# Optimization experiments

Hardware: AMD Instinct MI355X
Metric: run time of the kernel (lower is better)

The kernel has to match this reference:

```python
import jax, jax.numpy as jnp
import numpy as np

N_NODES = 50000   # field_size == number of graph nodes
N_EDGES = 800000  # avg degree 16
VOCAB = 200000    # feature_size
EMB = 64          # embedding_size == in_dim
HID = 64          # num_hidden
SLOPE = 0.2       # leaky relu negative slope


def setup_inputs() -> dict:
    key = jax.random.key(0)
    ks = jax.random.split(key, 20)
    s = 0.05
    d = {}
    d["features"] = jax.random.randint(ks[0], (8, N_NODES), 0, VOCAB, dtype=jnp.int32)
    d["feature_values"] = jax.random.uniform(ks[1], (8, N_NODES), dtype=jnp.float32)
    d["src"] = jax.random.randint(ks[2], (N_EDGES,), 0, N_NODES, dtype=jnp.int32)
    d["dst"] = jax.random.randint(ks[3], (N_EDGES,), 0, N_NODES, dtype=jnp.int32)
    d["emb"] = jax.random.normal(ks[4], (VOCAB, EMB), jnp.float32) * s
    # layer 0: in=64 -> heads=2, out=64 (no residual)
    d["W0"]  = jax.random.normal(ks[5], (EMB, 2 * HID), jnp.float32) * s
    d["al0"] = jax.random.normal(ks[6], (2, HID), jnp.float32) * s
    d["ar0"] = jax.random.normal(ks[7], (2, HID), jnp.float32) * s
    d["b0"]  = jnp.zeros((2 * HID,), jnp.float32)
    # layer 1: in=128 -> heads=2, out=64 (identity residual since in == heads*out)
    d["W1"]  = jax.random.normal(ks[8], (2 * HID, 2 * HID), jnp.float32) * s
    d["al1"] = jax.random.normal(ks[9], (2, HID), jnp.float32) * s
    d["ar1"] = jax.random.normal(ks[10], (2, HID), jnp.float32) * s
    d["b1"]  = jnp.zeros((2 * HID,), jnp.float32)
    # output layer: in=128 -> heads=1, out=64 (projected residual), no activation
    d["W2"]    = jax.random.normal(ks[11], (2 * HID, EMB), jnp.float32) * s
    d["al2"]   = jax.random.normal(ks[12], (1, EMB), jnp.float32) * s
    d["ar2"]   = jax.random.normal(ks[13], (1, EMB), jnp.float32) * s
    d["b2"]    = jnp.zeros((EMB,), jnp.float32)
    d["resW2"] = jax.random.normal(ks[14], (2 * HID, EMB), jnp.float32) * s
    return d


def _gat_layer(h, src, dst, W, al, ar, b, res, act):
    """DGL-style GATConv. h: [N, in], W: [in, H*D], al/ar: [H, D]."""
    N = h.shape[0]
    H, D = al.shape
    fh = (h @ W).reshape(N, H, D)                      # [N, H, D]
    el = jnp.einsum('nhd,hd->nh', fh, al)              # [N, H]
    er = jnp.einsum('nhd,hd->nh', fh, ar)              # [N, H]
    e = jax.nn.leaky_relu(el[src] + er[dst], SLOPE)    # [E, H]
    # edge softmax grouped by destination node
    m = jax.ops.segment_max(e, dst, num_segments=N)
    m = jnp.where(jnp.isfinite(m), m, 0.0)
    ex = jnp.exp(e - m[dst])
    den = jax.ops.segment_sum(ex, dst, num_segments=N)
    alpha = ex / jnp.maximum(den[dst], 1e-9)           # [E, H]
    out = jax.ops.segment_sum(alpha[:, :, None] * fh[src], dst, num_segments=N)  # [N, H, D]
    if res is not None:
        out = out + res
    out = out + b.reshape(H, D)
    if act:
        out = jax.nn.elu(out)
    return out


def reference(features, feature_values, src, dst, emb,
              W0, al0, ar0, b0, W1, al1, ar1, b1,
              W2, al2, ar2, b2, resW2):
    # embedding lookup scaled by feature values: [B, field, emb]
    fe = emb[features] * feature_values[..., None]
    h = fe[0]                                          # [N_NODES, EMB]
    # layer 0: no residual, elu, flatten heads
    h = _gat_layer(h, src, dst, W0, al0, ar0, b0, None, True).reshape(N_NODES, -1)
    # layer 1: identity residual (in == heads*out), elu, flatten heads
    res1 = h.reshape(N_NODES, 2, HID)
    h = _gat_layer(h, src, dst, W1, al1, ar1, b1, res1, True).reshape(N_NODES, -1)
    # output layer: projected residual, no activation, mean over heads
    res2 = (h @ resW2).reshape(N_NODES, 1, EMB)
    logits = _gat_layer(h, src, dst, W2, al2, ar2, b2, res2, False).mean(axis=1)
    return logits
```

## Files before the change

kernel.cpp:

```cpp
#include <hip/hip_runtime.h>
#include <hip/hip_fp16.h>


typedef __attribute__((ext_vector_type(8))) short short8;
typedef __attribute__((ext_vector_type(4))) float float4v;

__device__ __forceinline__ float lrelu(float x){ return fmaxf(x, 0.2f*x); }

__device__ __forceinline__ unsigned short f2bf(float f){
  unsigned int u = __float_as_uint(f);
  u += 0x7fffu + ((u >> 16) & 1u);
  return (unsigned short)(u >> 16);
}
__device__ __forceinline__ unsigned short f2h(float f){
  return __half_as_ushort(__float2half(f));
}
__device__ __forceinline__ int bperm(int idx, int v){
  return __builtin_amdgcn_ds_bpermute(idx, v);
}
__device__ __forceinline__ float bperm_f(int idx, int v){
  return __int_as_float(__builtin_amdgcn_ds_bpermute(idx, v));
}
__device__ __forceinline__ float elu1(float x){
  return x > 0.f ? x : (__expf(x) - 1.f);
}

__global__ void k_zero_i32(int* __restrict__ p, int n){
  int i = blockIdx.x*blockDim.x + threadIdx.x;
  if (i < n) p[i] = 0;
}

__global__ void k_hist_rank(const int* __restrict__ dst, int* __restrict__ counts,
                            int* __restrict__ rank, int E){
  int i = blockIdx.x*blockDim.x + threadIdx.x;
  if (i < E){
    int d = dst[i];
    rank[i] = atomicAdd(&counts[d], 1);
  }
}

__global__ void k_scan_local(const int* __restrict__ counts, int* __restrict__ row_ptr,
                             int* __restrict__ bsum, int N){
  __shared__ int s[256];
  int t = threadIdx.x, g = blockIdx.x*256 + t;
  int v = (g < N) ? counts[g] : 0;
  s[t] = v; __syncthreads();
  #pragma unroll
  for (int off = 1; off < 256; off <<= 1){
    int x = 0;
    if (t >= off) x = s[t-off];
    __syncthreads();
    s[t] += x;
    __syncthreads();
  }
  if (g < N) row_ptr[g+1] = s[t];
  if (g == 0 && t == 0) row_ptr[0] = 0;
  if (t == 255) bsum[blockIdx.x] = s[255];
}

__global__ void k_scan_top(int* __restrict__ bsum, int nb){
  __shared__ int s[256];
  int t = threadIdx.x;
  int v = (t < nb) ? bsum[t] : 0;
  s[t] = v; __syncthreads();
  #pragma unroll
  for (int off = 1; off < 256; off <<= 1){
    int x = 0;
    if (t >= off) x = s[t-off];
    __syncthreads();
    s[t] += x;
    __syncthreads();
  }
  if (t < nb) bsum[t] = s[t] - v;
}

__global__ void k_scan_fix(int* __restrict__ row_ptr, const int* __restrict__ bsum, int N){
  int g = blockIdx.x*256 + threadIdx.x;
  if (g < N && blockIdx.x > 0) row_ptr[g+1] += bsum[blockIdx.x];
}

__global__ void k_scatter2(const int* __restrict__ src, const int* __restrict__ dst,
                           const int* __restrict__ rank, const int* __restrict__ row_ptr,
                           int* __restrict__ ssrc, int E){
  int i = blockIdx.x*blockDim.x + threadIdx.x;
  if (i < E) ssrc[row_ptr[dst[i]] + rank[i]] = src[i];
}

__global__ void k_wprep_all(const float* __restrict__ W0, const float* __restrict__ W1,
                            const float* __restrict__ W2, const float* __restrict__ rW2,
                            unsigned short* __restrict__ Wt0, unsigned short* __restrict__ Wt1,
                            unsigned short* __restrict__ Wt2){
  int id = blockIdx.x*256 + threadIdx.x;
  if (id < 128*64){
    int n = id/64, k = id%64;
    Wt0[n*64 + k] = f2bf(W0[k*128 + n]);
  } else if (id < 128*64 + 128*128){
    int i = id - 128*64; int n = i/128, k = i%128;
    Wt1[n*128 + k] = f2bf(W1[k*128 + n]);
  } else if (id < 128*64 + 2*128*128){
    int i = id - 128*64 - 128*128; int n = i/128, k = i%128;
    float v = (n < 64) ? W2[k*64 + n] : rW2[k*64 + (n - 64)];
    Wt2[n*128 + k] = f2bf(v);
  }
}

template<int IN, int H, bool EMBED>
__global__ __launch_bounds__(256) void k_gemm_mfma(
    const unsigned short* __restrict__ hb,
    const int* __restrict__ feat, const float* __restrict__ fv,
    const float* __restrict__ embp,
    const unsigned short* __restrict__ Wt,
    const float* __restrict__ al, const float* __restrict__ ar,
    unsigned short* __restrict__ fhb,
    float* __restrict__ elr, int N){
  constexpr int KS = IN/32;
  constexpr int LDP = IN + 8;
  __shared__ unsigned short Wt_s[128*LDP];
  const int t = threadIdx.x;
  const int lane = t & 63, wid = t >> 6;
  const int l15 = lane & 15, quad = lane >> 4;
  const int row0 = blockIdx.x*64 + wid*16;

  for (int id = t; id < 128*(IN/8); id += 256){
    int r = id/(IN/8), seg = id%(IN/8);
    ((uint4*)(Wt_s + r*LDP))[seg] = ((const uint4*)(Wt + (size_t)r*IN))[seg];
  }
  short8 a[KS];
  int arow = row0 + l15;
  if (EMBED){
    if (arow < N){
      const float* er2 = embp + (size_t)feat[arow]*64;
      float sc = fv[arow];
      #pragma unroll
// ... 41 lines not shown
  }
  #pragma unroll
  for (int reg = 0; reg < 4; reg++){
    int row = row0 + quad*4 + reg;
    bool rv = row < N;
    if (rv){
      #pragma unroll
      for (int nt = 0; nt < 8; nt++)
        fhb[(size_t)row*128 + nt*16 + l15] = f2h(acc[nt][reg]);
    }
    float pel0 = 0.f, per0 = 0.f, pel1 = 0.f, per1 = 0.f;
    #pragma unroll
    for (int nt = 0; nt < 4; nt++){
      pel0 += acc[nt][reg]*alc[nt];     per0 += acc[nt][reg]*arc[nt];
      pel1 += acc[nt+4][reg]*alc[nt+4]; per1 += acc[nt+4][reg]*arc[nt+4];
    }
    #pragma unroll
    for (int off = 1; off < 16; off <<= 1){
      pel0 += __shfl_xor(pel0, off, 64);
      pel1 += __shfl_xor(pel1, off, 64);
      per0 += __shfl_xor(per0, off, 64);
      per1 += __shfl_xor(per1, off, 64);
    }
    if (l15 == 0 && rv){
      elr[row*4+0] = pel0;
      elr[row*4+1] = (H == 2) ? pel1 : 0.f;
      elr[row*4+2] = per0;
      elr[row*4+3] = (H == 2) ? per1 : 0.f;
    }
  }
}

template<int H>
__global__ __launch_bounds__(256) void k_agg(
    const unsigned short* __restrict__ fhb,
    const float* __restrict__ elr,
    const int* __restrict__ row_ptr, const int* __restrict__ ssrc,
    const float* __restrict__ bias, const float* __restrict__ res,
    int act, int res_from_fh,
    float* __restrict__ out, int out_ld, unsigned* __restrict__ outb, int N){
  int lane = threadIdx.x & 63, wid = threadIdx.x >> 6;
  int n = blockIdx.x*4 + wid;
  if (n >= N) return;
  int beg = row_ptr[n], end = row_ptr[n+1];
  float er0 = elr[n*4+2];
  float er1 = (H == 2) ? elr[n*4+3] : 0.f;

  const char* fhbB = (const char*)fhb;
  const int g  = (H == 2) ? (lane >> 4) : (lane >> 3);
  const int c  = (H == 2) ? (lane & 15) : (lane & 7);
  const unsigned cb = (unsigned)c << 4;
  const int hb4 = (H == 2 && c >= 8) ? (32 << 2) : 0;
  const int g4 = g << 2;

  float acc[8];
  #pragma unroll
  for (int k = 0; k < 8; k++) acc[k] = 0.f;
  float den0 = 0.f, den1 = 0.f;

  for (int base = beg; base < end; base += 64){
    int s = 0; float e0 = 0.f, e1 = 0.f;
    int i = base + lane;
    if (i < end){
      s = ssrc[i];
      float2 el = *(const float2*)(elr + s*4);
      e0 = __expf(fminf(lrelu(el.x + er0), 30.f));
      if (H == 2) e1 = __expf(fminf(lrelu(el.y + er1), 30.f));
      den0 += e0; den1 += e1;
    }
    int cnt = min(64, end - base);
    if (H == 2){
      float e1x = __shfl_xor(e1, 32, 64);
      float e0x = __shfl_xor(e0, 32, 64);
      int ap  = __float_as_int((lane < 32) ? e0  : e1x);
      int ap2 = __float_as_int((lane < 32) ? e0x : e1);
      for (int j0 = 0; j0 < cnt; j0 += 4){
        int apx = (j0 < 32) ? ap : ap2;
        int sj = bperm(((j0 + g) << 2), s);
        unsigned off = ((unsigned)sj << 8) + cb;
        uint4 w = *(const uint4*)(fhbB + off);
        float aj = bperm_f((((j0 & 31) + g) << 2) + hb4, apx);
        const __half2* hp = (const __half2*)&w;
        #pragma unroll
        for (int q = 0; q < 4; q++){
          acc[2*q]   = fmaf((float)hp[q].x, aj, acc[2*q]);
          acc[2*q+1] = fmaf((float)hp[q].y, aj, acc[2*q+1]);
        }
      }
    } else {
      int av = __float_as_int(e0);
      for (int j0 = 0; j0 < cnt; j0 += 8){
        int sj = bperm((j0 << 2) + g4, s);
        unsigned off = ((unsigned)sj << 8) + cb;
        uint4 w = *(const uint4*)(fhbB + off);
        float aj = bperm_f((j0 << 2) + g4, av);
        const __half2* hp = (const __half2*)&w;
        #pragma unroll
        for (int q = 0; q < 4; q++){
          acc[2*q]   = fmaf((float)hp[q].x, aj, acc[2*q]);
          acc[2*q+1] = fmaf((float)hp[q].y, aj, acc[2*q+1]);
        }
      }
    }
  }

  #pragma unroll
  for (int off = 32; off >= 1; off >>= 1){
    den0 += __shfl_xor(den0, off, 64);
    if (H == 2) den1 += __shfl_xor(den1, off, 64);
  }
  float rd0 = den0 > 0.f ? 1.f/den0 : 0.f;
  float rd1 = (H == 2 && den1 > 0.f) ? 1.f/den1 : 0.f;

  #pragma unroll
  for (int k = 0; k < 8; k++){
    if (H == 1) acc[k] += __shfl_xor(acc[k], 8, 64);
    acc[k] += __shfl_xor(acc[k], 16, 64);
    acc[k] += __shfl_xor(acc[k], 32, 64);
  }

  if (H == 2){
    if (lane < 16){
      int cc = lane;
      float rs = (cc < 8) ? rd0 : rd1;
      float o[8];
      const float4* b4 = (const float4*)bias;
      float4 ba = b4[cc*2], bb = b4[cc*2+1];
      o[0]=fmaf(acc[0],rs,ba.x); o[1]=fmaf(acc[1],rs,ba.y);
      o[2]=fmaf(acc[2],rs,ba.z); o[3]=fmaf(acc[3],rs,ba.w);
      o[4]=fmaf(acc[4],rs,bb.x); o[5]=fmaf(acc[5],rs,bb.y);
      o[6]=fmaf(acc[6],rs,bb.z); o[7]=fmaf(acc[7],rs,bb.w);
      if (res){
        const float4* r4 = (const float4*)(res + (size_t)n*128);
        float4 ra = r4[cc*2], rb = r4[cc*2+1];
        o[0]+=ra.x; o[1]+=ra.y; o[2]+=ra.z; o[3]+=ra.w;
        o[4]+=rb.x; o[5]+=rb.y; o[6]+=rb.z; o[7]+=rb.w;
      }
      if (act){
        #pragma unroll
        for (int k = 0; k < 8; k++) o[k] = elu1(o[k]);
      }
      if (out){
        float4* o4 = (float4*)(out + (size_t)n*out_ld);
        o4[cc*2]   = make_float4(o[0], o[1], o[2], o[3]);
        o4[cc*2+1] = make_float4(o[4], o[5], o[6], o[7]);
      }
      if (outb){
        uint4 ob;
        ob.x = (unsigned)f2bf(o[0]) | ((unsigned)f2bf(o[1]) << 16);
        ob.y = (unsigned)f2bf(o[2]) | ((unsigned)f2bf(o[3]) << 16);
        ob.z = (unsigned)f2bf(o[4]) | ((unsigned)f2bf(o[5]) << 16);
        ob.w = (unsigned)f2bf(o[6]) | ((unsigned)f2bf(o[7]) << 16);
        *(uint4*)(outb + (size_t)n*64 + cc*4) = ob;
      }
    }
  } else {
    if (lane < 8){
      int cc = lane;
      float o[8];
      #pragma unroll
      for (int k = 0; k < 8; k++) o[k] = fmaf(acc[k], rd0, bias[cc*8 + k]);
      if (res_from_fh){
        const uint4* fh4 = (const uint4*)fhb;
        uint4 r = fh4[(size_t)n*16 + 8 + cc];
        const __half2* rp = (const __half2*)&r;
        #pragma unroll
        for (int q = 0; q < 4; q++){
          o[2*q]   += (float)rp[q].x;
          o[2*q+1] += (float)rp[q].y;
        }
      }
      float4* o4 = (float4*)(out + (size_t)n*out_ld);
      o4[cc*2]   = make_float4(o[0], o[1], o[2], o[3]);
      o4[cc*2+1] = make_float4(o[4], o[5], o[6], o[7]);
    }
  }
}

extern "C" void kernel_launch(void* const* d_in, const int* in_sizes, int n_in,
                              void* d_out, int out_size, void* d_ws, size_t ws_size,
                              hipStream_t stream) {
  const int*   feat = (const int*)  d_in[0];
  const float* fv   = (const float*)d_in[1];
  const int*   src  = (const int*)  d_in[2];
  const int*   dst  = (const int*)  d_in[3];
  const float* emb  = (const float*)d_in[4];
  const float* W0   = (const float*)d_in[5];
  const float* al0  = (const float*)d_in[6];
  const float* ar0  = (const float*)d_in[7];
  const float* b0   = (const float*)d_in[8];
  const float* W1   = (const float*)d_in[9];
  const float* al1  = (const float*)d_in[10];
  const float* ar1  = (const float*)d_in[11];
  const float* b1   = (const float*)d_in[12];
  const float* W2   = (const float*)d_in[13];
  const float* al2  = (const float*)d_in[14];
  const float* ar2  = (const float*)d_in[15];
  const float* b2   = (const float*)d_in[16];
  const float* rW2  = (const float*)d_in[17];
  const int N = in_sizes[0] / 8;
  const int E = in_sizes[2];

  size_t off = 0;
  auto alloc = [&](size_t bytes) -> void* {
    void* p = (char*)d_ws + off;
    off = (off + bytes + 255) & ~(size_t)255;
    return p;
  };
  unsigned short* P1 = (unsigned short*)alloc((size_t)N*128*sizeof(unsigned short));
  float* P2     = (float*)alloc((size_t)N*128*sizeof(float));
  unsigned short* hb = (unsigned short*)alloc((size_t)N*128*sizeof(unsigned short));
  float* elr    = (float*)alloc((size_t)N*4*sizeof(float));
  int* row_ptr  = (int*)alloc((size_t)(N+1)*sizeof(int));
  int* counts   = (int*)alloc((size_t)N*sizeof(int));
  int* rank     = (int*)alloc((size_t)E*sizeof(int));
  int* ssrc     = (int*)alloc((size_t)E*sizeof(int));
  int* bsum     = (int*)alloc(256*sizeof(int));
  unsigned short* Wt0 = (unsigned short*)alloc((size_t)128*64*sizeof(unsigned short));
  unsigned short* Wt1 = (unsigned short*)alloc((size_t)128*128*sizeof(unsigned short));
  unsigned short* Wt2 = (unsigned short*)alloc((size_t)128*128*sizeof(unsigned short));

  int nb1 = (N + 255) / 256;
  k_zero_i32<<<(N + 255)/256, 256, 0, stream>>>(counts, N);
  k_hist_rank<<<(E + 255)/256, 256, 0, stream>>>(dst, counts, rank, E);
  k_scan_local<<<nb1, 256, 0, stream>>>(counts, row_ptr, bsum, N);
  k_scan_top<<<1, 256, 0, stream>>>(bsum, nb1);
  k_scan_fix<<<nb1, 256, 0, stream>>>(row_ptr, bsum, N);
  k_scatter2<<<(E + 255)/256, 256, 0, stream>>>(src, dst, rank, row_ptr, ssrc, E);
  k_wprep_all<<<(128*64 + 2*128*128 + 255)/256, 256, 0, stream>>>(
      W0, W1, W2, rW2, Wt0, Wt1, Wt2);

  int gt = (N + 63)/64;
  int nagg = (N + 3)/4;
  k_gemm_mfma<64,2,true><<<gt, 256, 0, stream>>>(nullptr, feat, fv, emb,
                                                 Wt0, al0, ar0, P1, elr, N);
  k_agg<2><<<nagg, 256, 0, stream>>>(P1, elr, row_ptr, ssrc, b0, nullptr,
                                     1, 0, P2, 128, (unsigned*)hb, N);
  k_gemm_mfma<128,2,false><<<gt, 256, 0, stream>>>(hb, nullptr, nullptr, nullptr,
                                                   Wt1, al1, ar1, P1, elr, N);
  k_agg<2><<<nagg, 256, 0, stream>>>(P1, elr, row_ptr, ssrc, b1, P2,
                                     1, 0, nullptr, 128, (unsigned*)hb, N);
  k_gemm_mfma<128,1,false><<<gt, 256, 0, stream>>>(hb, nullptr, nullptr, nullptr,
                                                   Wt2, al2, ar2, P1, elr, N);
  k_agg<1><<<nagg, 256, 0, stream>>>(P1, elr, row_ptr, ssrc, b2, nullptr,
                                     0, 1, (float*)d_out, 64, nullptr, N);
}
```

Measured before the change: 332.0 us.

## Split edge attention scores into separate per-edge kernel before aggregation

```diff
diff --git a/kernel.cpp b/kernel.cpp
--- a/kernel.cpp
+++ b/kernel.cpp
@@ -14,12 +14,6 @@
 }
 __device__ __forceinline__ unsigned short f2h(float f){
   return __half_as_ushort(__float2half(f));
-}
-__device__ __forceinline__ int bperm(int idx, int v){
-  return __builtin_amdgcn_ds_bpermute(idx, v);
-}
-__device__ __forceinline__ float bperm_f(int idx, int v){
-  return __int_as_float(__builtin_amdgcn_ds_bpermute(idx, v));
 }
 __device__ __forceinline__ float elu1(float x){
   return x > 0.f ? x : (__expf(x) - 1.f);
@@ -81,9 +75,14 @@
 
 __global__ void k_scatter2(const int* __restrict__ src, const int* __restrict__ dst,
                            const int* __restrict__ rank, const int* __restrict__ row_ptr,
-                           int* __restrict__ ssrc, int E){
+                           int* __restrict__ ssrc, int* __restrict__ sdst, int E){
   int i = blockIdx.x*blockDim.x + threadIdx.x;
-  if (i < E) ssrc[row_ptr[dst[i]] + rank[i]] = src[i];
+  if (i < E){
+    int d = dst[i];
+    int p = row_ptr[d] + rank[i];
+    ssrc[p] = src[i];
+    sdst[p] = d;
+  }
 }
 
 __global__ void k_wprep_all(const float* __restrict__ W0, const float* __restrict__ W1,
@@ -206,9 +205,29 @@
 }
 
 template<int H>
+__global__ __launch_bounds__(256) void k_alpha(
+    const float* __restrict__ elr, const int* __restrict__ ssrc,
+    const int* __restrict__ sdst, float* __restrict__ ealpha, int E){
+  int t = blockIdx.x*256 + threadIdx.x;
+  if (t >= E) return;
+  int s = ssrc[t], d = sdst[t];
+  if (H == 2){
+    float2 el = *(const float2*)(elr + s*4);
+    float2 er = *(const float2*)(elr + d*4 + 2);
+    float e0 = __expf(fminf(lrelu(el.x + er.x), 30.f));
+    float e1 = __expf(fminf(lrelu(el.y + er.y), 30.f));
+    ((float2*)ealpha)[t] = make_float2(e0, e1);
+  } else {
+    float el = elr[s*4];
+    float er = elr[d*4 + 2];
+    ealpha[t] = __expf(fminf(lrelu(el + er), 30.f));
+  }
+}
+
+template<int H>
 __global__ __launch_bounds__(256) void k_agg(
     const unsigned short* __restrict__ fhb,
-    const float* __restrict__ elr,
+    const float* __restrict__ ealpha,
     const int* __restrict__ row_ptr, const int* __restrict__ ssrc,
     const float* __restrict__ bias, const float* __restrict__ res,
     int act, int res_from_fh,
@@ -217,67 +236,16 @@
   int n = blockIdx.x*4 + wid;
   if (n >= N) return;
   int beg = row_ptr[n], end = row_ptr[n+1];
-  float er0 = elr[n*4+2];
-  float er1 = (H == 2) ? elr[n*4+3] : 0.f;
-
-  const char* fhbB = (const char*)fhb;
-  const int g  = (H == 2) ? (lane >> 4) : (lane >> 3);
-  const int c  = (H == 2) ? (lane & 15) : (lane & 7);
-  const unsigned cb = (unsigned)c << 4;
-  const int hb4 = (H == 2 && c >= 8) ? (32 << 2) : 0;
-  const int g4 = g << 2;
-
-  float acc[8];
-  #pragma unroll
-  for (int k = 0; k < 8; k++) acc[k] = 0.f;
+
   float den0 = 0.f, den1 = 0.f;
-
-  for (int base = beg; base < end; base += 64){
-    int s = 0; float e0 = 0.f, e1 = 0.f;
-    int i = base + lane;
-    if (i < end){
-      s = ssrc[i];
-      float2 el = *(const float2*)(elr + s*4);
-      e0 = __expf(fminf(lrelu(el.x + er0), 30.f));
-      if (H == 2) e1 = __expf(fminf(lrelu(el.y + er1), 30.f));
-      den0 += e0; den1 += e1;
-    }
-    int cnt = min(64, end - base);
-    if (H == 2){
-      float e1x = __shfl_xor(e1, 32, 64);
-      float e0x = __shfl_xor(e0, 32, 64);
-      int ap  = __float_as_int((lane < 32) ? e0  : e1x);
-      int ap2 = __float_as_int((lane < 32) ? e0x : e1);
-      for (int j0 = 0; j0 < cnt; j0 += 4){
-        int apx = (j0 < 32) ? ap : ap2;
-        int sj = bperm(((j0 + g) << 2), s);
-        unsigned off = ((unsigned)sj << 8) + cb;
-        uint4 w = *(const uint4*)(fhbB + off);
-        float aj = bperm_f((((j0 & 31) + g) << 2) + hb4, apx);
-        const __half2* hp = (const __half2*)&w;
-        #pragma unroll
-        for (int q = 0; q < 4; q++){
-          acc[2*q]   = fmaf((float)hp[q].x, aj, acc[2*q]);
-          acc[2*q+1] = fmaf((float)hp[q].y, aj, acc[2*q+1]);
-        }
-      }
-    } else {
-      int av = __float_as_int(e0);
-      for (int j0 = 0; j0 < cnt; j0 += 8){
-        int sj = bperm((j0 << 2) + g4, s);
-        unsigned off = ((unsigned)sj << 8) + cb;
-        uint4 w = *(const uint4*)(fhbB + off);
-        float aj = bperm_f((j0 << 2) + g4, av);
-        const __half2* hp = (const __half2*)&w;
-        #pragma unroll
-        for (int q = 0; q < 4; q++){
-          acc[2*q]   = fmaf((float)hp[q].x, aj, acc[2*q]);
-          acc[2*q+1] = fmaf((float)hp[q].y, aj, acc[2*q+1]);
-        }
-      }
-    }
-  }
-
+  if (H == 2){
+    for (int i = beg + lane; i < end; i += 64){
+      float2 ea = ((const float2*)ealpha)[i];
+      den0 += ea.x; den1 += ea.y;
+    }
+  } else {
+    for (int i = beg + lane; i < end; i += 64) den0 += ealpha[i];
+  }
   #pragma unroll
   for (int off = 32; off >= 1; off >>= 1){
     den0 += __shfl_xor(den0, off, 64);
@@ -285,6 +253,63 @@
   }
   float rd0 = den0 > 0.f ? 1.f/den0 : 0.f;
   float rd1 = (H == 2 && den1 > 0.f) ? 1.f/den1 : 0.f;
+
+  const char* fhbB = (const char*)fhb;
+  constexpr int GS = (H == 2) ? 4 : 8;
+  const int g = (H == 2) ? (lane >> 4) : (lane >> 3);
+  const int c = (H == 2) ? (lane & 15) : (lane & 7);
+  const unsigned cb = (unsigned)c << 4;
+  const bool hi = (H == 2) && (c >= 8);
+
+  float acc[8];
+  #pragma unroll
+  for (int k = 0; k < 8; k++) acc[k] = 0.f;
+
+  int deg = end - beg;
+  int j = g;
+  for (; j + GS < deg; j += 2*GS){
+    int i0 = beg + j, i1 = beg + j + GS;
+    int s0 = ssrc[i0], s1 = ssrc[i1];
+    float a0, a1;
+    if (H == 2){
+      float2 ea0 = ((const float2*)ealpha)[i0];
+      float2 ea1 = ((const float2*)ealpha)[i1];
+      a0 = hi ? ea0.y : ea0.x;
+      a1 = hi ? ea1.y : ea1.x;
+    } else {
+      a0 = ealpha[i0]; a1 = ealpha[i1];
+    }
+    uint4 w0 = *(const uint4*)(fhbB + (((unsigned)s0 << 8) + cb));
+    uint4 w1 = *(const uint4*)(fhbB + (((unsigned)s1 << 8) + cb));
+    const __half2* h0 = (const __half2*)&w0;
+    const __half2* h1 = (const __half2*)&w1;
+    #pragma unroll
+    for (int q = 0; q < 4; q++){
+      acc[2*q]   = fmaf((float)h0[q].x, a0, acc[2*q]);
+      acc[2*q+1] = fmaf((float)h0[q].y, a0, acc[2*q+1]);
+    }
+    #pragma unroll
+    for (int q = 0; q < 4; q++){
+      acc[2*q]   = fmaf((float)h1[q].x, a1, acc[2*q]);
+      acc[2*q+1] = fmaf((float)h1[q].y, a1, acc[2*q+1]);
+    }
+  }
+  if (j < deg){
+    int i0 = beg + j;
+    int s0 = ssrc[i0];
+    float a0;
+    if (H == 2){
+      float2 ea0 = ((const float2*)ealpha)[i0];
+      a0 = hi ? ea0.y : ea0.x;
+    } else a0 = ealpha[i0];
+    uint4 w0 = *(const uint4*)(fhbB + (((unsigned)s0 << 8) + cb));
+    const __half2* h0 = (const __half2*)&w0;
+    #pragma unroll
+    for (int q = 0; q < 4; q++){
+      acc[2*q]   = fmaf((float)h0[q].x, a0, acc[2*q]);
+      acc[2*q+1] = fmaf((float)h0[q].y, a0, acc[2*q+1]);
+    }
+  }
 
   #pragma unroll
   for (int k = 0; k < 8; k++){
@@ -389,18 +414,21 @@
   int* counts   = (int*)alloc((size_t)N*sizeof(int));
   int* rank     = (int*)alloc((size_t)E*sizeof(int));
   int* ssrc     = (int*)alloc((size_t)E*sizeof(int));
+  int* sdst     = (int*)alloc((size_t)E*sizeof(int));
+  float* ealpha = (float*)alloc((size_t)E*2*sizeof(float));
   int* bsum     = (int*)alloc(256*sizeof(int));
   unsigned short* Wt0 = (unsigned short*)alloc((size_t)128*64*sizeof(unsigned short));
   unsigned short* Wt1 = (unsigned short*)alloc((size_t)128*128*sizeof(unsigned short));
   unsigned short* Wt2 = (unsigned short*)alloc((size_t)128*128*sizeof(unsigned short));
 
   int nb1 = (N + 255) / 256;
+  int eb  = (E + 255) / 256;
   k_zero_i32<<<(N + 255)/256, 256, 0, stream>>>(counts, N);
-  k_hist_rank<<<(E + 255)/256, 256, 0, stream>>>(dst, counts, rank, E);
+  k_hist_rank<<<eb, 256, 0, stream>>>(dst, counts, rank, E);
   k_scan_local<<<nb1, 256, 0, stream>>>(counts, row_ptr, bsum, N);
   k_scan_top<<<1, 256, 0, stream>>>(bsum, nb1);
   k_scan_fix<<<nb1, 256, 0, stream>>>(row_ptr, bsum, N);
-  k_scatter2<<<(E + 255)/256, 256, 0, stream>>>(src, dst, rank, row_ptr, ssrc, E);
+  k_scatter2<<<eb, 256, 0, stream>>>(src, dst, rank, row_ptr, ssrc, sdst, E);
   k_wprep_all<<<(128*64 + 2*128*128 + 255)/256, 256, 0, stream>>>(
       W0, W1, W2, rW2, Wt0, Wt1, Wt2);
 
@@ -408,14 +436,17 @@
   int nagg = (N + 3)/4;
   k_gemm_mfma<64,2,true><<<gt, 256, 0, stream>>>(nullptr, feat, fv, emb,
                                                  Wt0, al0, ar0, P1, elr, N);
-  k_agg<2><<<nagg, 256, 0, stream>>>(P1, elr, row_ptr, ssrc, b0, nullptr,
+  k_alpha<2><<<eb, 256, 0, stream>>>(elr, ssrc, sdst, ealpha, E);
+  k_agg<2><<<nagg, 256, 0, stream>>>(P1, ealpha, row_ptr, ssrc, b0, nullptr,
                                      1, 0, P2, 128, (unsigned*)hb, N);
   k_gemm_mfma<128,2,false><<<gt, 256, 0, stream>>>(hb, nullptr, nullptr, nullptr,
                                                    Wt1, al1, ar1, P1, elr, N);
-  k_agg<2><<<nagg, 256, 0, stream>>>(P1, elr, row_ptr, ssrc, b1, P2,
+  k_alpha<2><<<eb, 256, 0, stream>>>(elr, ssrc, sdst, ealpha, E);
+  k_agg<2><<<nagg, 256, 0, stream>>>(P1, ealpha, row_ptr, ssrc, b1, P2,
                                      1, 0, nullptr, 128, (unsigned*)hb, N);
   k_gemm_mfma<128,1,false><<<gt, 256, 0, stream>>>(hb, nullptr, nullptr, nullptr,
                                                    Wt2, al2, ar2, P1, elr, N);
-  k_agg<1><<<nagg, 256, 0, stream>>>(P1, elr, row_ptr, ssrc, b2, nullptr,
+  k_alpha<1><<<eb, 256, 0, stream>>>(elr, ssrc, sdst, ealpha, E);
+  k_agg<1><<<nagg, 256, 0, stream>>>(P1, ealpha, row_ptr, ssrc, b2, nullptr,
                                      0, 1, (float*)d_out, 64, nullptr, N);
 }
```

Result: slower. 360.5 us (+8.6%).

## Switch aggregation to edge-balanced blocks with shared-memory atomic accumulation

Applied to the files above, without the earlier changes.

```diff
diff --git a/kernel.cpp b/kernel.cpp
--- a/kernel.cpp
+++ b/kernel.cpp
@@ -14,12 +14,6 @@
 }
 __device__ __forceinline__ unsigned short f2h(float f){
   return __half_as_ushort(__float2half(f));
-}
-__device__ __forceinline__ int bperm(int idx, int v){
-  return __builtin_amdgcn_ds_bpermute(idx, v);
-}
-__device__ __forceinline__ float bperm_f(int idx, int v){
-  return __int_as_float(__builtin_amdgcn_ds_bpermute(idx, v));
 }
 __device__ __forceinline__ float elu1(float x){
   return x > 0.f ? x : (__expf(x) - 1.f);
@@ -81,9 +75,14 @@
 
 __global__ void k_scatter2(const int* __restrict__ src, const int* __restrict__ dst,
                            const int* __restrict__ rank, const int* __restrict__ row_ptr,
-                           int* __restrict__ ssrc, int E){
+                           int* __restrict__ ssrc, int* __restrict__ sdst, int E){
   int i = blockIdx.x*blockDim.x + threadIdx.x;
-  if (i < E) ssrc[row_ptr[dst[i]] + rank[i]] = src[i];
+  if (i < E){
+    int d = dst[i];
+    int p = row_ptr[d] + rank[i];
+    ssrc[p] = src[i];
+    sdst[p] = d;
+  }
 }
 
 __global__ void k_wprep_all(const float* __restrict__ W0, const float* __restrict__ W1,
@@ -206,147 +205,128 @@
 }
 
 template<int H>
-__global__ __launch_bounds__(256) void k_agg(
+__global__ __launch_bounds__(256) void k_agg_em(
     const unsigned short* __restrict__ fhb,
     const float* __restrict__ elr,
     const int* __restrict__ row_ptr, const int* __restrict__ ssrc,
+    const int* __restrict__ sdst,
     const float* __restrict__ bias, const float* __restrict__ res,
     int act, int res_from_fh,
     float* __restrict__ out, int out_ld, unsigned* __restrict__ outb, int N){
-  int lane = threadIdx.x & 63, wid = threadIdx.x >> 6;
-  int n = blockIdx.x*4 + wid;
-  if (n >= N) return;
-  int beg = row_ptr[n], end = row_ptr[n+1];
-  float er0 = elr[n*4+2];
-  float er1 = (H == 2) ? elr[n*4+3] : 0.f;
+  constexpr int NB = 64;
+  constexpr int NC = (H == 2) ? 128 : 64;
+  constexpr int PC = (H == 2) ? 8 : 4;
+  __shared__ float acc_s[NB*NC];
+  __shared__ float den_s[NB*2];
+  const int t = threadIdx.x;
+  const int n0 = blockIdx.x*NB;
+  const int ncnt = min(NB, N - n0);
+
+  for (int i = t; i < NB*NC; i += 256) acc_s[i] = 0.f;
+  if (t < NB*2) den_s[t] = 0.f;
+  __syncthreads();
+
+  const int ebeg = row_ptr[n0];
+  const int eend = row_ptr[n0 + ncnt];
+  const int gq = t >> 4, c = t & 15;
+  const int chunk = (eend - ebeg + 15) >> 4;
+  const int gb = ebeg + gq*chunk;
+  const int ge = min(gb + chunk, eend);
 
   const char* fhbB = (const char*)fhb;
-  const int g  = (H == 2) ? (lane >> 4) : (lane >> 3);
-  const int c  = (H == 2) ? (lane & 15) : (lane & 7);
-  const unsigned cb = (unsigned)c << 4;
-  const int hb4 = (H == 2 && c >= 8) ? (32 << 2) : 0;
-  const int g4 = g << 2;
-
-  float acc[8];
-  #pragma unroll
-  for (int k = 0; k < 8; k++) acc[k] = 0.f;
-  float den0 = 0.f, den1 = 0.f;
-
-  for (int base = beg; base < end; base += 64){
-    int s = 0; float e0 = 0.f, e1 = 0.f;
-    int i = base + lane;
-    if (i < end){
-      s = ssrc[i];
+  const unsigned cb = (H == 2) ? ((unsigned)c << 4) : ((unsigned)c << 3);
+
+  float racc[PC];
+  #pragma unroll
+  for (int k = 0; k < PC; k++) racc[k] = 0.f;
+  float rden0 = 0.f, rden1 = 0.f;
+  int dcur = -1; float er0 = 0.f, er1 = 0.f;
+
+  for (int i = gb; i < ge; i++){
+    int s = ssrc[i], d = sdst[i];
+    if (d != dcur){
+      if (dcur >= 0){
+        float* ap = acc_s + (dcur - n0)*NC + c*PC;
+        #pragma unroll
+        for (int k = 0; k < PC; k++){ atomicAdd(&ap[k], racc[k]); racc[k] = 0.f; }
+        if (c == 0) atomicAdd(&den_s[(dcur - n0)*2 + 0], rden0);
+        if (H == 2 && c == 1) atomicAdd(&den_s[(dcur - n0)*2 + 1], rden1);
+        rden0 = 0.f; rden1 = 0.f;
+      }
+      dcur = d;
+      if (H == 2){
+        float2 er = *(const float2*)(elr + d*4 + 2); er0 = er.x; er1 = er.y;
+      } else er0 = elr[d*4 + 2];
+    }
+    float e0, e1 = 0.f;
+    if (H == 2){
       float2 el = *(const float2*)(elr + s*4);
       e0 = __expf(fminf(lrelu(el.x + er0), 30.f));
-      if (H == 2) e1 = __expf(fminf(lrelu(el.y + er1), 30.f));
-      den0 += e0; den1 += e1;
-    }
-    int cnt = min(64, end - base);
+      e1 = __expf(fminf(lrelu(el.y + er1), 30.f));
+    } else {
+      e0 = __expf(fminf(lrelu(elr[s*4] + er0), 30.f));
+    }
+    rden0 += e0; rden1 += e1;
     if (H == 2){
-      float e1x = __shfl_xor(e1, 32, 64);
-      float e0x = __shfl_xor(e0, 32, 64);
-      int ap  = __float_as_int((lane < 32) ? e0  : e1x);
-      int ap2 = __float_as_int((lane < 32) ? e0x : e1);
-      for (int j0 = 0; j0 < cnt; j0 += 4){
-        int apx = (j0 < 32) ? ap : ap2;
-        int sj = bperm(((j0 + g) << 2), s);
-        unsigned off = ((unsigned)sj << 8) + cb;
-        uint4 w = *(const uint4*)(fhbB + off);
-        float aj = bperm_f((((j0 & 31) + g) << 2) + hb4, apx);
-        const __half2* hp = (const __half2*)&w;
-        #pragma unroll
-        for (int q = 0; q < 4; q++){
-          acc[2*q]   = fmaf((float)hp[q].x, aj, acc[2*q]);
-          acc[2*q+1] = fmaf((float)hp[q].y, aj, acc[2*q+1]);
-        }
+      uint4 w = *(const uint4*)(fhbB + (((unsigned)s << 8) + cb));
+      float a = (c < 8) ? e0 : e1;
+      const __half2* hp = (const __half2*)&w;
+      #pragma unroll
+      for (int q = 0; q < 4; q++){
+        racc[2*q]   = fmaf((float)hp[q].x, a, racc[2*q]);
+        racc[2*q+1] = fmaf((float)hp[q].y, a, racc[2*q+1]);
       }
     } else {
-      int av = __float_as_int(e0);
-      for (int j0 = 0; j0 < cnt; j0 += 8){
-        int sj = bperm((j0 << 2) + g4, s);
-        unsigned off = ((unsigned)sj << 8) + cb;
-        uint4 w = *(const uint4*)(fhbB + off);
-        float aj = bperm_f((j0 << 2) + g4, av);
-        const __half2* hp = (const __half2*)&w;
-        #pragma unroll
-        for (int q = 0; q < 4; q++){
-          acc[2*q]   = fmaf((float)hp[q].x, aj, acc[2*q]);
-          acc[2*q+1] = fmaf((float)hp[q].y, aj, acc[2*q+1]);
-        }
+      uint2 w = *(const uint2*)(fhbB + (((unsigned)s << 8) + cb));
+      const __half2* hp = (const __half2*)&w;
+      #pragma unroll
+      for (int q = 0; q < 2; q++){
+        racc[2*q]   = fmaf((float)hp[q].x, e0, racc[2*q]);
+        racc[2*q+1] = fmaf((float)hp[q].y, e0, racc[2*q+1]);
       }
     }
   }
-
-  #pragma unroll
-  for (int off = 32; off >= 1; off >>= 1){
-    den0 += __shfl_xor(den0, off, 64);
-    if (H == 2) den1 += __shfl_xor(den1, off, 64);
-  }
-  float rd0 = den0 > 0.f ? 1.f/den0 : 0.f;
-  float rd1 = (H == 2 && den1 > 0.f) ? 1.f/den1 : 0.f;
-
-  #pragma unroll
-  for (int k = 0; k < 8; k++){
-    if (H == 1) acc[k] += __shfl_xor(acc[k], 8, 64);
-    acc[k] += __shfl_xor(acc[k], 16, 64);
-    acc[k] += __shfl_xor(acc[k], 32, 64);
-  }
-
-  if (H == 2){
-    if (lane < 16){
-      int cc = lane;
-      float rs = (cc < 8) ? rd0 : rd1;
-      float o[8];
-      const float4* b4 = (const float4*)bias;
-      float4 ba = b4[cc*2], bb = b4[cc*2+1];
-      o[0]=fmaf(acc[0],rs,ba.x); o[1]=fmaf(acc[1],rs,ba.y);
-      o[2]=fmaf(acc[2],rs,ba.z); o[3]=fmaf(acc[3],rs,ba.w);
-      o[4]=fmaf(acc[4],rs,bb.x); o[5]=fmaf(acc[5],rs,bb.y);
-      o[6]=fmaf(acc[6],rs,bb.z); o[7]=fmaf(acc[7],rs,bb.w);
-      if (res){
-        const float4* r4 = (const float4*)(res + (size_t)n*128);
-        float4 ra = r4[cc*2], rb = r4[cc*2+1];
-        o[0]+=ra.x; o[1]+=ra.y; o[2]+=ra.z; o[3]+=ra.w;
-        o[4]+=rb.x; o[5]+=rb.y; o[6]+=rb.z; o[7]+=rb.w;
-      }
-      if (act){
-        #pragma unroll
-        for (int k = 0; k < 8; k++) o[k] = elu1(o[k]);
-      }
-      if (out){
-        float4* o4 = (float4*)(out + (size_t)n*out_ld);
-        o4[cc*2]   = make_float4(o[0], o[1], o[2], o[3]);
-        o4[cc*2+1] = make_float4(o[4], o[5], o[6], o[7]);
-      }
-      if (outb){
-        uint4 ob;
-        ob.x = (unsigned)f2bf(o[0]) | ((unsigned)f2bf(o[1]) << 16);
-        ob.y = (unsigned)f2bf(o[2]) | ((unsigned)f2bf(o[3]) << 16);
-        ob.z = (unsigned)f2bf(o[4]) | ((unsigned)f2bf(o[5]) << 16);
-        ob.w = (unsigned)f2bf(o[6]) | ((unsigned)f2bf(o[7]) << 16);
-        *(uint4*)(outb + (size_t)n*64 + cc*4) = ob;
-      }
-    }
-  } else {
-    if (lane < 8){
-      int cc = lane;
-      float o[8];
-      #pragma unroll
-      for (int k = 0; k < 8; k++) o[k] = fmaf(acc[k], rd0, bias[cc*8 + k]);
-      if (res_from_fh){
-        const uint4* fh4 = (const uint4*)fhb;
-        uint4 r = fh4[(size_t)n*16 + 8 + cc];
-        const __half2* rp = (const __half2*)&r;
-        #pragma unroll
-        for (int q = 0; q < 4; q++){
-          o[2*q]   += (float)rp[q].x;
-          o[2*q+1] += (float)rp[q].y;
-        }
-      }
-      float4* o4 = (float4*)(out + (size_t)n*out_ld);
-      o4[cc*2]   = make_float4(o[0], o[1], o[2], o[3]);
-      o4[cc*2+1] = make_float4(o[4], o[5], o[6], o[7]);
+  if (dcur >= 0){
+    float* ap = acc_s + (dcur - n0)*NC + c*PC;
+    #pragma unroll
+    for (int k = 0; k < PC; k++) atomicAdd(&ap[k], racc[k]);
+    if (c == 0) atomicAdd(&den_s[(dcur - n0)*2 + 0], rden0);
+    if (H == 2 && c == 1) atomicAdd(&den_s[(dcur - n0)*2 + 1], rden1);
+  }
+  __syncthreads();
+
+  for (int idx = t; idx < ncnt*(NC/4); idx += 256){
+    int ld = idx/(NC/4), p = idx%(NC/4);
+    int n = n0 + ld, col0 = p*4;
+    float dn0 = den_s[ld*2], dn1 = den_s[ld*2+1];
+    float rs;
+    if (H == 2) rs = (col0 < 64) ? (dn0 > 0.f ? 1.f/dn0 : 0.f)
+                                 : (dn1 > 0.f ? 1.f/dn1 : 0.f);
+    else        rs = dn0 > 0.f ? 1.f/dn0 : 0.f;
+    float o[4];
+    #pragma unroll
+    for (int q = 0; q < 4; q++) o[q] = fmaf(acc_s[ld*NC + col0 + q], rs, bias[col0 + q]);
+    if (H == 2 && res){
+      float4 rv = *(const float4*)(res + (size_t)n*128 + col0);
+      o[0] += rv.x; o[1] += rv.y; o[2] += rv.z; o[3] += rv.w;
+    }
+    if (H == 1 && res_from_fh){
+      uint2 r = *(const uint2*)(fhbB + (size_t)n*256 + 128 + col0*2);
+      const __half2* rp = (const __half2*)&r;
+      o[0] += (float)rp[0].x; o[1] += (float)rp[0].y;
+      o[2] += (float)rp[1].x; o[3] += (float)rp[1].y;
+    }
+    if (act){
+      #pragma unroll
+      for (int q = 0; q < 4; q++) o[q] = elu1(o[q]);
+    }
+    if (out) *(float4*)(out + (size_t)n*out_ld + col0) =
+        make_float4(o[0], o[1], o[2], o[3]);
+    if (outb){
+      uint2 ob;
+      ob.x = (unsigned)f2bf(o[0]) | ((unsigned)f2bf(o[1]) << 16);
+      ob.y = (unsigned)f2bf(o[2]) | ((unsigned)f2bf(o[3]) << 16);
+      *(uint2*)(outb + (size_t)n*64 + (col0 >> 1)) = ob;
     }
   }
 }
@@ -389,33 +369,35 @@
   int* counts   = (int*)alloc((size_t)N*sizeof(int));
   int* rank     = (int*)alloc((size_t)E*sizeof(int));
   int* ssrc     = (int*)alloc((size_t)E*sizeof(int));
+  int* sdst     = (int*)alloc((size_t)E*sizeof(int));
   int* bsum     = (int*)alloc(256*sizeof(int));
   unsigned short* Wt0 = (unsigned short*)alloc((size_t)128*64*sizeof(unsigned short));
   unsigned short* Wt1 = (unsigned short*)alloc((size_t)128*128*sizeof(unsigned short));
   unsigned short* Wt2 = (unsigned short*)alloc((size_t)128*128*sizeof(unsigned short));
 
   int nb1 = (N + 255) / 256;
+  int eb  = (E + 255) / 256;
   k_zero_i32<<<(N + 255)/256, 256, 0, stream>>>(counts, N);
-  k_hist_rank<<<(E + 255)/256, 256, 0, stream>>>(dst, counts, rank, E);
+  k_hist_rank<<<eb, 256, 0, stream>>>(dst, counts, rank, E);
   k_scan_local<<<nb1, 256, 0, stream>>>(counts, row_ptr, bsum, N);
   k_scan_top<<<1, 256, 0, stream>>>(bsum, nb1);
   k_scan_fix<<<nb1, 256, 0, stream>>>(row_ptr, bsum, N);
-  k_scatter2<<<(E + 255)/256, 256, 0, stream>>>(src, dst, rank, row_ptr, ssrc, E);
+  k_scatter2<<<eb, 256, 0, stream>>>(src, dst, rank, row_ptr, ssrc, sdst, E);
   k_wprep_all<<<(128*64 + 2*128*128 + 255)/256, 256, 0, stream>>>(
       W0, W1, W2, rW2, Wt0, Wt1, Wt2);
 
-  int gt = (N + 63)/64;
-  int nagg = (N + 3)/4;
+  int gt  = (N + 63)/64;
+  int nem = (N + 63)/64;
   k_gemm_mfma<64,2,true><<<gt, 256, 0, stream>>>(nullptr, feat, fv, emb,
                                                  Wt0, al0, ar0, P1, elr, N);
-  k_agg<2><<<nagg, 256, 0, stream>>>(P1, elr, row_ptr, ssrc, b0, nullptr,
-                                     1, 0, P2, 128, (unsigned*)hb, N);
+  k_agg_em<2><<<nem, 256, 0, stream>>>(P1, elr, row_ptr, ssrc, sdst, b0, nullptr,
+                                       1, 0, P2, 128, (unsigned*)hb, N);
   k_gemm_mfma<128,2,false><<<gt, 256, 0, stream>>>(hb, nullptr, nullptr, nullptr,
                                                    Wt1, al1, ar1, P1, elr, N);
-  k_agg<2><<<nagg, 256, 0, stream>>>(P1, elr, row_ptr, ssrc, b1, P2,
-                                     1, 0, nullptr, 128, (unsigned*)hb, N);
+  k_agg_em<2><<<nem, 256, 0, stream>>>(P1, elr, row_ptr, ssrc, sdst, b1, P2,
+                                       1, 0, nullptr, 128, (unsigned*)hb, N);
   k_gemm_mfma<128,1,false><<<gt, 256, 0, stream>>>(hb, nullptr, nullptr, nullptr,
                                                    Wt2, al2, ar2, P1, elr, N);
-  k_agg<1><<<nagg, 256, 0, stream>>>(P1, elr, row_ptr, ssrc, b2, nullptr,
-                                     0, 1, (float*)d_out, 64, nullptr, N);
-}
+  k_agg_em<1><<<nem, 256, 0, stream>>>(P1, elr, row_ptr, ssrc, sdst, b2, nullptr,
+                                       0, 1, (float*)d_out, 64, nullptr, N);
+}
```

Measured after the change: 440.3 us. 1.33x slower.

## Aggregate each node with a 16-lane group instead of a full wavefront

Applied to the files above, without the earlier changes.

```diff
diff --git a/kernel.cpp b/kernel.cpp
--- a/kernel.cpp
+++ b/kernel.cpp
@@ -15,19 +15,8 @@
 __device__ __forceinline__ unsigned short f2h(float f){
   return __half_as_ushort(__float2half(f));
 }
-__device__ __forceinline__ int bperm(int idx, int v){
-  return __builtin_amdgcn_ds_bpermute(idx, v);
-}
-__device__ __forceinline__ float bperm_f(int idx, int v){
-  return __int_as_float(__builtin_amdgcn_ds_bpermute(idx, v));
-}
 __device__ __forceinline__ float elu1(float x){
   return x > 0.f ? x : (__expf(x) - 1.f);
-}
-
-__global__ void k_zero_i32(int* __restrict__ p, int n){
-  int i = blockIdx.x*blockDim.x + threadIdx.x;
-  if (i < n) p[i] = 0;
 }
 
 __global__ void k_hist_rank(const int* __restrict__ dst, int* __restrict__ counts,
@@ -86,19 +75,22 @@
   if (i < E) ssrc[row_ptr[dst[i]] + rank[i]] = src[i];
 }
 
-__global__ void k_wprep_all(const float* __restrict__ W0, const float* __restrict__ W1,
-                            const float* __restrict__ W2, const float* __restrict__ rW2,
-                            unsigned short* __restrict__ Wt0, unsigned short* __restrict__ Wt1,
-                            unsigned short* __restrict__ Wt2){
+__global__ void k_setup(int* __restrict__ counts, int N,
+                        const float* __restrict__ W0, const float* __restrict__ W1,
+                        const float* __restrict__ W2, const float* __restrict__ rW2,
+                        unsigned short* __restrict__ Wt0, unsigned short* __restrict__ Wt1,
+                        unsigned short* __restrict__ Wt2){
   int id = blockIdx.x*256 + threadIdx.x;
-  if (id < 128*64){
-    int n = id/64, k = id%64;
+  if (id < N){ counts[id] = 0; return; }
+  int j = id - N;
+  if (j < 128*64){
+    int n = j/64, k = j%64;
     Wt0[n*64 + k] = f2bf(W0[k*128 + n]);
-  } else if (id < 128*64 + 128*128){
-    int i = id - 128*64; int n = i/128, k = i%128;
+  } else if (j < 128*64 + 128*128){
+    int i = j - 128*64; int n = i/128, k = i%128;
     Wt1[n*128 + k] = f2bf(W1[k*128 + n]);
-  } else if (id < 128*64 + 2*128*128){
-    int i = id - 128*64 - 128*128; int n = i/128, k = i%128;
+  } else if (j < 128*64 + 2*128*128){
+    int i = j - 128*64 - 128*128; int n = i/128, k = i%128;
     float v = (n < 64) ? W2[k*64 + n] : rW2[k*64 + (n - 64)];
     Wt2[n*128 + k] = f2bf(v);
   }
@@ -206,148 +198,153 @@
 }
 
 template<int H>
-__global__ __launch_bounds__(256) void k_agg(
+__global__ __launch_bounds__(256) void k_agg_gp(
     const unsigned short* __restrict__ fhb,
     const float* __restrict__ elr,
     const int* __restrict__ row_ptr, const int* __restrict__ ssrc,
     const float* __restrict__ bias, const float* __restrict__ res,
     int act, int res_from_fh,
     float* __restrict__ out, int out_ld, unsigned* __restrict__ outb, int N){
-  int lane = threadIdx.x & 63, wid = threadIdx.x >> 6;
-  int n = blockIdx.x*4 + wid;
+  const int t = threadIdx.x;
+  const int gq = t >> 4, c = t & 15;
+  const int n = blockIdx.x*16 + gq;
   if (n >= N) return;
-  int beg = row_ptr[n], end = row_ptr[n+1];
-  float er0 = elr[n*4+2];
-  float er1 = (H == 2) ? elr[n*4+3] : 0.f;
+  const int beg = row_ptr[n], end = row_ptr[n+1];
+  const float er0 = elr[n*4+2];
+  const float er1 = (H == 2) ? elr[n*4+3] : 0.f;
 
   const char* fhbB = (const char*)fhb;
-  const int g  = (H == 2) ? (lane >> 4) : (lane >> 3);
-  const int c  = (H == 2) ? (lane & 15) : (lane & 7);
-  const unsigned cb = (unsigned)c << 4;
-  const int hb4 = (H == 2 && c >= 8) ? (32 << 2) : 0;
-  const int g4 = g << 2;
-
-  float acc[8];
-  #pragma unroll
-  for (int k = 0; k < 8; k++) acc[k] = 0.f;
+  const unsigned cb = (H == 2) ? ((unsigned)c << 4) : ((unsigned)c << 3);
+  constexpr int PC = (H == 2) ? 8 : 4;
+
+  float acc[PC];
+  #pragma unroll
+  for (int k = 0; k < PC; k++) acc[k] = 0.f;
   float den0 = 0.f, den1 = 0.f;
 
-  for (int base = beg; base < end; base += 64){
-    int s = 0; float e0 = 0.f, e1 = 0.f;
-    int i = base + lane;
-    if (i < end){
-      s = ssrc[i];
-      float2 el = *(const float2*)(elr + s*4);
-      e0 = __expf(fminf(lrelu(el.x + er0), 30.f));
-      if (H == 2) e1 = __expf(fminf(lrelu(el.y + er1), 30.f));
-      den0 += e0; den1 += e1;
-    }
-    int cnt = min(64, end - base);
+  int i = beg;
+  for (; i + 1 < end; i += 2){
+    int s0 = ssrc[i], s1 = ssrc[i+1];
+    float2 el0 = *(const float2*)(elr + s0*4);
+    float2 el1 = *(const float2*)(elr + s1*4);
+    float e00 = __expf(fminf(lrelu(el0.x + er0), 30.f));
+    float e10 = __expf(fminf(lrelu(el1.x + er0), 30.f));
+    float e01 = 0.f, e11 = 0.f;
     if (H == 2){
-      float e1x = __shfl_xor(e1, 32, 64);
-      float e0x = __shfl_xor(e0, 32, 64);
-      int ap  = __float_as_int((lane < 32) ? e0  : e1x);
-      int ap2 = __float_as_int((lane < 32) ? e0x : e1);
-      for (int j0 = 0; j0 < cnt; j0 += 4){
-        int apx = (j0 < 32) ? ap : ap2;
-        int sj = bperm(((j0 + g) << 2), s);
-        unsigned off = ((unsigned)sj << 8) + cb;
-        uint4 w = *(const uint4*)(fhbB + off);
-        float aj = bperm_f((((j0 & 31) + g) << 2) + hb4, apx);
-        const __half2* hp = (const __half2*)&w;
-        #pragma unroll
-        for (int q = 0; q < 4; q++){
-          acc[2*q]   = fmaf((float)hp[q].x, aj, acc[2*q]);
-          acc[2*q+1] = fmaf((float)hp[q].y, aj, acc[2*q+1]);
-        }
+      e01 = __expf(fminf(lrelu(el0.y + er1), 30.f));
+      e11 = __expf(fminf(lrelu(el1.y + er1), 30.f));
+    }
+    den0 += e00 + e10; den1 += e01 + e11;
+    if (H == 2){
+      uint4 w0 = *(const uint4*)(fhbB + (((unsigned)s0 << 8) + cb));
+      uint4 w1 = *(const uint4*)(fhbB + (((unsigned)s1 << 8) + cb));
+      float a0 = (c < 8) ? e00 : e01;
+      float a1 = (c < 8) ? e10 : e11;
+      const __half2* h0 = (const __half2*)&w0;
+      const __half2* h1 = (const __half2*)&w1;
+      #pragma unroll
+      for (int q = 0; q < 4; q++){
+        acc[2*q]   = fmaf((float)h0[q].x, a0, acc[2*q]);
+        acc[2*q+1] = fmaf((float)h0[q].y, a0, acc[2*q+1]);
+      }
+      #pragma unroll
+      for (int q = 0; q < 4; q++){
+        acc[2*q]   = fmaf((float)h1[q].x, a1, acc[2*q]);
+        acc[2*q+1] = fmaf((float)h1[q].y, a1, acc[2*q+1]);
       }
     } else {
-      int av = __float_as_int(e0);
-      for (int j0 = 0; j0 < cnt; j0 += 8){
-        int sj = bperm((j0 << 2) + g4, s);
-        unsigned off = ((unsigned)sj << 8) + cb;
-        uint4 w = *(const uint4*)(fhbB + off);
-        float aj = bperm_f((j0 << 2) + g4, av);
-        const __half2* hp = (const __half2*)&w;
-        #pragma unroll
-        for (int q = 0; q < 4; q++){
-          acc[2*q]   = fmaf((float)hp[q].x, aj, acc[2*q]);
-          acc[2*q+1] = fmaf((float)hp[q].y, aj, acc[2*q+1]);
-        }
-      }
-    }
-  }
-
-  #pragma unroll
-  for (int off = 32; off >= 1; off >>= 1){
-    den0 += __shfl_xor(den0, off, 64);
-    if (H == 2) den1 += __shfl_xor(den1, off, 64);
-  }
+      uint2 w0 = *(const uint2*)(fhbB + (((unsigned)s0 << 8) + cb));
+      uint2 w1 = *(const uint2*)(fhbB + (((unsigned)s1 << 8) + cb));
+      const __half2* h0 = (const __half2*)&w0;
+      const __half2* h1 = (const __half2*)&w1;
+      #pragma unroll
+      for (int q = 0; q < 2; q++){
+        acc[2*q]   = fmaf((float)h0[q].x, e00, acc[2*q]);
+        acc[2*q+1] = fmaf((float)h0[q].y, e00, acc[2*q+1]);
+      }
+      #pragma unroll
+      for (int q = 0; q < 2; q++){
+        acc[2*q]   = fmaf((float)h1[q].x, e10, acc[2*q]);
+        acc[2*q+1] = fmaf((float)h1[q].y, e10, acc[2*q+1]);
+      }
+    }
+  }
+  if (i < end){
+    int s0 = ssrc[i];
+    float2 el0 = *(const float2*)(elr + s0*4);
+    float e00 = __expf(fminf(lrelu(el0.x + er0), 30.f));
+    float e01 = (H == 2) ? __expf(fminf(lrelu(el0.y + er1), 30.f)) : 0.f;
+    den0 += e00; den1 += e01;
+    if (H == 2){
+      uint4 w0 = *(const uint4*)(fhbB + (((unsigned)s0 << 8) + cb));
+      float a0 = (c < 8) ? e00 : e01;
+      const __half2* h0 = (const __half2*)&w0;
+      #pragma unroll
+      for (int q = 0; q < 4; q++){
+        acc[2*q]   = fmaf((float)h0[q].x, a0, acc[2*q]);
+        acc[2*q+1] = fmaf((float)h0[q].y, a0, acc[2*q+1]);
+      }
+    } else {
+      uint2 w0 = *(const uint2*)(fhbB + (((unsigned)s0 << 8) + cb));
+      const __half2* h0 = (const __half2*)&w0;
+      #pragma unroll
+      for (int q = 0; q < 2; q++){
+        acc[2*q]   = fmaf((float)h0[q].x, e00, acc[2*q]);
+        acc[2*q+1] = fmaf((float)h0[q].y, e00, acc[2*q+1]);
+      }
+    }
+  }
+
   float rd0 = den0 > 0.f ? 1.f/den0 : 0.f;
   float rd1 = (H == 2 && den1 > 0.f) ? 1.f/den1 : 0.f;
 
-  #pragma unroll
-  for (int k = 0; k < 8; k++){
-    if (H == 1) acc[k] += __shfl_xor(acc[k], 8, 64);
-    acc[k] += __shfl_xor(acc[k], 16, 64);
-    acc[k] += __shfl_xor(acc[k], 32, 64);
-  }
-
   if (H == 2){
-    if (lane < 16){
-      int cc = lane;
-      float rs = (cc < 8) ? rd0 : rd1;
-      float o[8];
-      const float4* b4 = (const float4*)bias;
-      float4 ba = b4[cc*2], bb = b4[cc*2+1];
-      o[0]=fmaf(acc[0],rs,ba.x); o[1]=fmaf(acc[1],rs,ba.y);
-      o[2]=fmaf(acc[2],rs,ba.z); o[3]=fmaf(acc[3],rs,ba.w);
-      o[4]=fmaf(acc[4],rs,bb.x); o[5]=fmaf(acc[5],rs,bb.y);
-      o[6]=fmaf(acc[6],rs,bb.z); o[7]=fmaf(acc[7],rs,bb.w);
-      if (res){
-        const float4* r4 = (const float4*)(res + (size_t)n*128);
-        float4 ra = r4[cc*2], rb = r4[cc*2+1];
-        o[0]+=ra.x; o[1]+=ra.y; o[2]+=ra.z; o[3]+=ra.w;
-        o[4]+=rb.x; o[5]+=rb.y; o[6]+=rb.z; o[7]+=rb.w;
-      }
-      if (act){
-        #pragma unroll
-        for (int k = 0; k < 8; k++) o[k] = elu1(o[k]);
-      }
-      if (out){
-        float4* o4 = (float4*)(out + (size_t)n*out_ld);
-        o4[cc*2]   = make_float4(o[0], o[1], o[2], o[3]);
-        o4[cc*2+1] = make_float4(o[4], o[5], o[6], o[7]);
-      }
-      if (outb){
-        uint4 ob;
-        ob.x = (unsigned)f2bf(o[0]) | ((unsigned)f2bf(o[1]) << 16);
-        ob.y = (unsigned)f2bf(o[2]) | ((unsigned)f2bf(o[3]) << 16);
-        ob.z = (unsigned)f2bf(o[4]) | ((unsigned)f2bf(o[5]) << 16);
-        ob.w = (unsigned)f2bf(o[6]) | ((unsigned)f2bf(o[7]) << 16);
-        *(uint4*)(outb + (size_t)n*64 + cc*4) = ob;
-      }
+    float rs = (c < 8) ? rd0 : rd1;
+    float o[8];
+    const float4* b4 = (const float4*)(bias + c*8);
+    float4 ba = b4[0], bb = b4[1];
+    o[0]=fmaf(acc[0],rs,ba.x); o[1]=fmaf(acc[1],rs,ba.y);
+    o[2]=fmaf(acc[2],rs,ba.z); o[3]=fmaf(acc[3],rs,ba.w);
+    o[4]=fmaf(acc[4],rs,bb.x); o[5]=fmaf(acc[5],rs,bb.y);
+    o[6]=fmaf(acc[6],rs,bb.z); o[7]=fmaf(acc[7],rs,bb.w);
+    if (res){
+      const float4* r4 = (const float4*)(res + (size_t)n*128 + c*8);
+      float4 ra = r4[0], rb = r4[1];
+      o[0]+=ra.x; o[1]+=ra.y; o[2]+=ra.z; o[3]+=ra.w;
+      o[4]+=rb.x; o[5]+=rb.y; o[6]+=rb.z; o[7]+=rb.w;
+    }
+    if (act){
+      #pragma unroll
+      for (int k = 0; k < 8; k++) o[k] = elu1(o[k]);
+    }
+    if (out){
+      float4* o4 = (float4*)(out + (size_t)n*out_ld + c*8);
+      o4[0] = make_float4(o[0], o[1], o[2], o[3]);
+      o4[1] = make_float4(o[4], o[5], o[6], o[7]);
+    }
+    if (outb){
+      uint4 ob;
+      ob.x = (unsigned)f2bf(o[0]) | ((unsigned)f2bf(o[1]) << 16);
+      ob.y = (unsigned)f2bf(o[2]) | ((unsigned)f2bf(o[3]) << 16);
+      ob.z = (unsigned)f2bf(o[4]) | ((unsigned)f2bf(o[5]) << 16);
+      ob.w = (unsigned)f2bf(o[6]) | ((unsigned)f2bf(o[7]) << 16);
+      *(uint4*)(outb + (size_t)n*64 + c*4) = ob;
     }
   } else {
-    if (lane < 8){
-      int cc = lane;
-      float o[8];
-      #pragma unroll
-      for (int k = 0; k < 8; k++) o[k] = fmaf(acc[k], rd0, bias[cc*8 + k]);
-      if (res_from_fh){
-        const uint4* fh4 = (const uint4*)fhb;
-        uint4 r = fh4[(size_t)n*16 + 8 + cc];
-        const __half2* rp = (const __half2*)&r;
-        #pragma unroll
-        for (int q = 0; q < 4; q++){
-          o[2*q]   += (float)rp[q].x;
-          o[2*q+1] += (float)rp[q].y;
-        }
-      }
-      float4* o4 = (float4*)(out + (size_t)n*out_ld);
-      o4[cc*2]   = make_float4(o[0], o[1], o[2], o[3]);
-      o4[cc*2+1] = make_float4(o[4], o[5], o[6], o[7]);
-    }
+    float o[4];
+    #pragma unroll
+    for (int k = 0; k < 4; k++) o[k] = fmaf(acc[k], rd0, bias[c*4 + k]);
+    if (res_from_fh){
+      uint2 r = *(const uint2*)(fhbB + (size_t)n*256 + 128 + c*8);
+      const __half2* rp = (const __half2*)&r;
+      o[0] += (float)rp[0].x; o[1] += (float)rp[0].y;
+      o[2] += (float)rp[1].x; o[3] += (float)rp[1].y;
+    }
+    if (act){
+      #pragma unroll
+      for (int k = 0; k < 4; k++) o[k] = elu1(o[k]);
+    }
+    *(float4*)(out + (size_t)n*out_ld + c*4) = make_float4(o[0], o[1], o[2], o[3]);
   }
 }
 
@@ -395,27 +392,27 @@
   unsigned short* Wt2 = (unsigned short*)alloc((size_t)128*128*sizeof(unsigned short));
 
   int nb1 = (N + 255) / 256;
-  k_zero_i32<<<(N + 255)/256, 256, 0, stream>>>(counts, N);
-  k_hist_rank<<<(E + 255)/256, 256, 0, stream>>>(dst, counts, rank, E);
+  int eb  = (E + 255) / 256;
+  k_setup<<<(N + 128*64 + 2*128*128 + 255)/256, 256, 0, stream>>>(
+      counts, N, W0, W1, W2, rW2, Wt0, Wt1, Wt2);
+  k_hist_rank<<<eb, 256, 0, stream>>>(dst, counts, rank, E);
   k_scan_local<<<nb1, 256, 0, stream>>>(counts, row_ptr, bsum, N);
   k_scan_top<<<1, 256, 0, stream>>>(bsum, nb1);
   k_scan_fix<<<nb1, 256, 0, stream>>>(row_ptr, bsum, N);
-  k_scatter2<<<(E + 255)/256, 256, 0, stream>>>(src, dst, rank, row_ptr, ssrc, E);
-  k_wprep_all<<<(128*64 + 2*128*128 + 255)/256, 256, 0, stream>>>(
-      W0, W1, W2, rW2, Wt0, Wt1, Wt2);
-
-  int gt = (N + 63)/64;
-  int nagg = (N + 3)/4;
+  k_scatter2<<<eb, 256, 0, stream>>>(src, dst, rank, row_ptr, ssrc, E);
+
+  int gt  = (N + 63)/64;
+  int ngp = (N + 15)/16;
   k_gemm_mfma<64,2,true><<<gt, 256, 0, stream>>>(nullptr, feat, fv, emb,
                                                  Wt0, al0, ar0, P1, elr, N);
-  k_agg<2><<<nagg, 256, 0, stream>>>(P1, elr, row_ptr, ssrc, b0, nullptr,
-                                     1, 0, P2, 128, (unsigned*)hb, N);
+  k_agg_gp<2><<<ngp, 256, 0, stream>>>(P1, elr, row_ptr, ssrc, b0, nullptr,
+                                       1, 0, P2, 128, (unsigned*)hb, N);
   k_gemm_mfma<128,2,false><<<gt, 256, 0, stream>>>(hb, nullptr, nullptr, nullptr,
                                                    Wt1, al1, ar1, P1, elr, N);
-  k_agg<2><<<nagg, 256, 0, stream>>>(P1, elr, row_ptr, ssrc, b1, P2,
-                                     1, 0, nullptr, 128, (unsigned*)hb, N);
+  k_agg_gp<2><<<ngp, 256, 0, stream>>>(P1, elr, row_ptr, ssrc, b1, P2,
+                                       1, 0, nullptr, 128, (unsigned*)hb, N);
   k_gemm_mfma<128,1,false><<<gt, 256, 0, stream>>>(hb, nullptr, nullptr, nullptr,
                                                    Wt2, al2, ar2, P1, elr, N);
-  k_agg<1><<<nagg, 256, 0, stream>>>(P1, elr, row_ptr, ssrc, b2, nullptr,
-                                     0, 1, (float*)d_out, 64, nullptr, N);
-}
+  k_agg_gp<1><<<ngp, 256, 0, stream>>>(P1, elr, row_ptr, ssrc, b2, nullptr,
+                                       0, 1, (float*)d_out, 64, nullptr, N);
+}
```

After: 322.0 us. -3.0%, faster.
